# Performance work log

Measured on AMD Instinct MI355X. Metric: run time of the kernel, lower is better.

Reference implementation:

```python
import jax, jax.numpy as jnp
import numpy as np

B, H, L, C = 16, 512, 4096, 1
LAM = 0.001  # kernel squash threshold (lam in LongConvKernel)


def setup_inputs() -> dict:
    key = jax.random.key(0)
    ks = jax.random.split(key, 5)
    u = jax.random.normal(ks[0], (B, H, L), jnp.float32)
    # LongConvKernel 'double_exp' init: K ~ N(0, 0.02^2) * exp(-(j/L) * (H//2)^(i/H))
    K = jax.random.normal(ks[1], (C, H, L), jnp.float32) * 0.02
    i = jnp.arange(H, dtype=jnp.float32)[:, None]
    j = jnp.arange(L, dtype=jnp.float32)[None, :]
    double_exp = jnp.exp(-(j / L) * jnp.power(float(H // 2), i / H))  # (H, L)
    kernel = K * double_exp[None]
    D = jax.random.normal(ks[2], (C, H), jnp.float32)  # skip connection params
    # TransposedLinear(C*H -> H): weight (d_output, d_input), kaiming-ish scale
    Wout = jax.random.normal(ks[3], (H, C * H), jnp.float32) / np.sqrt(C * H)
    bout = jax.random.normal(ks[4], (H,), jnp.float32) * 0.01
    return {"u": u, "kernel": kernel, "D": D, "Wout": Wout, "bout": bout}


def reference(u, kernel, D, Wout, bout):
    Lseq = u.shape[-1]
    # kernel squashing: relu(|k| - lam) * sign(k)  (soft-threshold)
    k = jax.nn.relu(jnp.abs(kernel) - LAM) * jnp.sign(kernel)  # (C, H, L)
    n = 2 * Lseq
    k_f = jnp.fft.rfft(k, n=n, axis=-1)            # (C, H, n//2+1) complex
    u_f = jnp.fft.rfft(u, n=n, axis=-1)            # (B, H, n//2+1) complex
    y_f = jnp.einsum('bhl,chl->bchl', u_f, k_f)    # pointwise multiply in freq
    y = jnp.fft.irfft(y_f, n=n, axis=-1)[..., :Lseq]  # (B, C, H, L)
    y = y + jnp.einsum('bhl,ch->bchl', u, D)       # skip term
    y = y.reshape(y.shape[0], C * H, Lseq)         # (B, C*H, L)
    y = jax.nn.gelu(y, approximate=False)          # activation (torch GELU = exact)
    # output_linear: TransposedLinear + swish postact
    y = jnp.einsum('bul,vu->bvl', y, Wout) + bout[None, :, None]
    y = jax.nn.silu(y)
    return y
```

## Files before the change

### kernel.cpp

```cpp
#include <hip/hip_runtime.h>
#include <hip/hip_bf16.h>
#include <math.h>

#define BB 16
#define HH 512
#define LL 4096
#define NFFT 8192
#define LAM 0.001f

typedef __attribute__((ext_vector_type(8))) short short8;
typedef __attribute__((ext_vector_type(4))) float floatx4;

__device__ __forceinline__ void cmul(float ar, float ai, float br, float bi,
                                     float& cr, float& ci) {
  cr = ar * br - ai * bi;
  ci = ar * bi + ai * br;
}

constexpr float W16C[10] = {1.f, 0.92387953f, 0.70710678f, 0.38268343f, 0.f,
                            -0.38268343f, -0.70710678f, -0.92387953f, -1.f, -0.92387953f};
constexpr float W16S[10] = {0.f, -0.38268343f, -0.70710678f, -0.92387953f, -1.f,
                            -0.92387953f, -0.70710678f, -0.38268343f, 0.f, 0.38268343f};
constexpr float W32C[16] = {1.f, 0.98078528f, 0.92387953f, 0.83146961f, 0.70710678f,
                            0.55557023f, 0.38268343f, 0.19509032f, 0.f, -0.19509032f,
                            -0.38268343f, -0.55557023f, -0.70710678f, -0.83146961f,
                            -0.92387953f, -0.98078528f};
constexpr float W32S[16] = {0.f, -0.19509032f, -0.38268343f, -0.55557023f, -0.70710678f,
                            -0.83146961f, -0.92387953f, -0.98078528f, -1.f, -0.98078528f,
                            -0.92387953f, -0.83146961f, -0.70710678f, -0.55557023f,
                            -0.38268343f, -0.19509032f};

__device__ __forceinline__ void fft16_f(float* xr, float* xi) {
  float yr[16], yi[16];
#pragma unroll
  for (int j = 0; j < 4; ++j) {
    float t0r = xr[j] + xr[j + 8],      t0i = xi[j] + xi[j + 8];
    float t1r = xr[j] - xr[j + 8],      t1i = xi[j] - xi[j + 8];
    float t2r = xr[j + 4] + xr[j + 12], t2i = xi[j + 4] + xi[j + 12];
    float t3r = xr[j + 4] - xr[j + 12], t3i = xi[j + 4] - xi[j + 12];
    float o0r = t0r + t2r, o0i = t0i + t2i;
    float o1r = t1r + t3i, o1i = t1i - t3r;
    float o2r = t0r - t2r, o2i = t0i - t2i;
    float o3r = t1r - t3i, o3i = t1i + t3r;
    yr[j] = o0r; yi[j] = o0i;
    if (j == 0) {
      yr[4] = o1r; yi[4] = o1i; yr[8] = o2r; yi[8] = o2i; yr[12] = o3r; yi[12] = o3i;
    } else {
      cmul(o1r, o1i, W16C[j], W16S[j], yr[j + 4], yi[j + 4]);
      cmul(o2r, o2i, W16C[2 * j], W16S[2 * j], yr[j + 8], yi[j + 8]);
      cmul(o3r, o3i, W16C[3 * j], W16S[3 * j], yr[j + 12], yi[j + 12]);
    }
  }
#pragma unroll
  for (int m = 0; m < 4; ++m) {
    float t0r = yr[4 * m] + yr[4 * m + 2],     t0i = yi[4 * m] + yi[4 * m + 2];
    float t1r = yr[4 * m] - yr[4 * m + 2],     t1i = yi[4 * m] - yi[4 * m + 2];
    float t2r = yr[4 * m + 1] + yr[4 * m + 3], t2i = yi[4 * m + 1] + yi[4 * m + 3];
    float t3r = yr[4 * m + 1] - yr[4 * m + 3], t3i = yi[4 * m + 1] - yi[4 * m + 3];
    xr[m] = t0r + t2r;       xi[m] = t0i + t2i;
    xr[m + 4] = t1r + t3i;   xi[m + 4] = t1i - t3r;
    xr[m + 8] = t0r - t2r;   xi[m + 8] = t0i - t2i;
    xr[m + 12] = t1r - t3i;  xi[m + 12] = t1i + t3r;
  }
}

__device__ __forceinline__ void ifft16_f(float* xr, float* xi) {
  float yr[16], yi[16];
#pragma unroll
  for (int m = 0; m < 4; ++m) {
    float t0r = xr[m] + xr[m + 8],      t0i = xi[m] + xi[m + 8];
    float t1r = xr[m] - xr[m + 8],      t1i = xi[m] - xi[m + 8];
    float t2r = xr[m + 4] + xr[m + 12], t2i = xi[m + 4] + xi[m + 12];
    float t3r = xr[m + 4] - xr[m + 12], t3i = xi[m + 4] - xi[m + 12];
    yr[4 * m] = t0r + t2r;     yi[4 * m] = t0i + t2i;
    yr[4 * m + 1] = t1r - t3i; yi[4 * m + 1] = t1i + t3r;
    yr[4 * m + 2] = t0r - t2r; yi[4 * m + 2] = t0i - t2i;
    yr[4 * m + 3] = t1r + t3i; yi[4 * m + 3] = t1i - t3r;
  }
#pragma unroll
  for (int j = 0; j < 4; ++j) {
    float v0r = yr[j], v0i = yi[j];
    float v1r, v1i, v2r, v2i, v3r, v3i;
    if (j == 0) {
      v1r = yr[4]; v1i = yi[4]; v2r = yr[8]; v2i = yi[8]; v3r = yr[12]; v3i = yi[12];
    } else {
      cmul(yr[j + 4], yi[j + 4], W16C[j], -W16S[j], v1r, v1i);
      cmul(yr[j + 8], yi[j + 8], W16C[2 * j], -W16S[2 * j], v2r, v2i);
      cmul(yr[j + 12], yi[j + 12], W16C[3 * j], -W16S[3 * j], v3r, v3i);
    }
    float t0r = v0r + v2r, t0i = v0i + v2i;
    float t1r = v0r - v2r, t1i = v0i - v2i;
    float t2r = v1r + v3r, t2i = v1i + v3i;
    float t3r = v1r - v3r, t3i = v1i - v3i;
    xr[j] = t0r + t2r;       xi[j] = t0i + t2i;
    xr[j + 4] = t1r - t3i;   xi[j + 4] = t1i + t3r;
    xr[j + 8] = t0r - t2r;   xi[j + 8] = t0i - t2i;
    xr[j + 12] = t1r + t3i;  xi[j + 12] = t1i - t3r;
  }
}

__device__ __forceinline__ void twtree(float ang, float* wc, float* ws) {
  wc[0] = 1.f; ws[0] = 0.f;
  __sincosf(ang, &ws[1], &wc[1]);
  cmul(wc[1], ws[1], wc[1], ws[1], wc[2], ws[2]);
  cmul(wc[1], ws[1], wc[2], ws[2], wc[3], ws[3]);
  cmul(wc[2], ws[2], wc[2], ws[2], wc[4], ws[4]);
  cmul(wc[1], ws[1], wc[4], ws[4], wc[5], ws[5]);
  cmul(wc[2], ws[2], wc[4], ws[4], wc[6], ws[6]);
  cmul(wc[3], ws[3], wc[4], ws[4], wc[7], ws[7]);
  cmul(wc[4], ws[4], wc[4], ws[4], wc[8], ws[8]);
#pragma unroll
  for (int m = 9; m < 16; ++m)
    cmul(wc[m - 8], ws[m - 8], wc[8], ws[8], wc[m], ws[m]);
}

__device__ __forceinline__ float gelu_exact(float y) {
  return 0.5f * y * (1.f + erff(y * 0.70710678118654752f));
}

__global__ void wconv_kernel(const float* __restrict__ W,
                             __hip_bfloat16* __restrict__ Wb) {
  int i = blockIdx.x * 256 + threadIdx.x;
  Wb[i] = __float2bfloat16(W[i]);
}

__global__ __launch_bounds__(512)
__attribute__((amdgpu_waves_per_eu(4, 4)))
void kf_kernel(const float* __restrict__ kern, float* __restrict__ Kf) {
  __shared__ __align__(16) float sre[NFFT];
  __shared__ __align__(16) float sim[NFFT];
  const int t = threadIdx.x;
  const int h = blockIdx.x;
  const float* kr = kern + (size_t)h * LL;

  {
    const int j = t;
    float xr[16], xi[16];
#pragma unroll
    for (int r = 0; r < 8; ++r) {
      float kv = kr[j + 512 * r];
      float a = fabsf(kv) - LAM;
      float sq = (a > 0.f) ? ((kv > 0.f) ? a : -a) : 0.f;
      xr[r] = sq * (1.0f / (float)NFFT);
      xi[r] = 0.f;
    }
#pragma unroll
    for (int r = 8; r < 16; ++r) { xr[r] = 0.f; xi[r] = 0.f; }
    fft16_f(xr, xi);
    float wc[16], ws[16];
    twtree(-6.283185307179586f * (float)j * (1.f / 8192.f), wc, ws);
    const int jx = j ^ (((j >> 5) & 7) << 2);
#pragma unroll
    for (int m = 0; m < 16; ++m) {
      float tr, ti; cmul(xr[m], xi[m], wc[m], ws[m], tr, ti);
      sre[jx + 512 * m] = tr; sim[jx + 512 * m] = ti;
    }
  }
  __syncthreads();

  {
    const int jj = t & 31, gg = t >> 5;
    const int base = gg * 512 + jj;
    float xr[16], xi[16];
#pragma unroll
    for (int m = 0; m < 16; ++m) {
      const int a = (base + 32 * m) ^ ((m & 7) << 2);
      xr[m] = sre[a]; xi[m] = sim[a];
    }
    fft16_f(xr, xi);
    float wc[16], ws[16];
    twtree(-6.283185307179586f * (float)jj * (1.f / 512.f), wc, ws);
#pragma unroll
    for (int m = 0; m < 16; ++m) {
      const int a = (base + 32 * m) ^ ((m & 7) << 2);
      float tr, ti; cmul(xr[m], xi[m], wc[m], ws[m], tr, ti);
      sre[a] = tr; sim[a] = ti;
    }
  }
  __syncthreads();

  {
    const int k = t >> 1, par = t & 1;
    const int kx = k & 7;
    const float sgn = par ? -1.f : 1.f;
    float xr[16], xi[16];
#pragma unroll
    for (int c = 0; c < 4; ++c) {
      float4 lr = ((const float4*)sre)[8 * k + (c ^ kx)];
      float4 hr = ((const float4*)sre)[8 * k + ((c + 4) ^ kx)];
      float4 li = ((const float4*)sim)[8 * k + (c ^ kx)];
      float4 hi4 = ((const float4*)sim)[8 * k + ((c + 4) ^ kx)];
      float vr[4] = {lr.x + sgn * hr.x, lr.y + sgn * hr.y, lr.z + sgn * hr.z, lr.w + sgn * hr.w};
      float vi[4] = {li.x + sgn * hi4.x, li.y + sgn * hi4.y, li.z + sgn * hi4.z, li.w + sgn * hi4.w};
#pragma unroll
      for (int e = 0; e < 4; ++e) {
        const int j = 4 * c + e;
        const float twr = par ? W32C[j] : 1.f;
        const float tws = par ? W32S[j] : 0.f;
        cmul(vr[e], vi[e], twr, tws, xr[j], xi[j]);
      }
    }
    fft16_f(xr, xi);
    float4* out4 = (float4*)(Kf + (size_t)h * NFFT * 2) + 8 * t;
#pragma unroll
    for (int c = 0; c < 8; ++c)
      out4[c] = make_float4(xr[2 * c], xi[2 * c], xr[2 * c + 1], xi[2 * c + 1]);
  }
}

__global__ __launch_bounds__(512)
__attribute__((amdgpu_waves_per_eu(4, 4)))
void fftconv_kernel(
    const float* __restrict__ u, const float* __restrict__ D,
    const float* __restrict__ Kf, __hip_bfloat16* __restrict__ g) {
  __shared__ __align__(16) float sre[NFFT];
  __shared__ __align__(16) float sim[NFFT];
  const int t = threadIdx.x;
  const int h = blockIdx.x;
  const int p = blockIdx.y;
  const int b0 = 2 * p, b1 = 2 * p + 1;
  const float* u0 = u + ((size_t)(b0 * HH + h)) * LL;
  const float* u1 = u + ((size_t)(b1 * HH + h)) * LL;

  float us0[8], us1[8];
  const int jx = t ^ (((t >> 5) & 7) << 2);

  {
    const int j = t;
    float xr[16], xi[16];
#pragma unroll
    for (int r = 0; r < 8; ++r) {
      float a = u0[j + 512 * r];
      float b = u1[j + 512 * r];
      us0[r] = a; us1[r] = b;
      xr[r] = a; xi[r] = b;
    }
#pragma unroll
    for (int r = 8; r < 16; ++r) { xr[r] = 0.f; xi[r] = 0.f; }
    fft16_f(xr, xi);
    float wc[16], ws[16];
    twtree(-6.283185307179586f * (float)j * (1.f / 8192.f), wc, ws);
#pragma unroll
    for (int m = 0; m < 16; ++m) {
      float tr, ti; cmul(xr[m], xi[m], wc[m], ws[m], tr, ti);
      sre[jx + 512 * m] = tr; sim[jx + 512 * m] = ti;
    }
  }
  __syncthreads();

  {
    const int jj = t & 31, gg = t >> 5;
    const int base = gg * 512 + jj;
    float xr[16], xi[16];
#pragma unroll
    for (int m = 0; m < 16; ++m) {
      const int a = (base + 32 * m) ^ ((m & 7) << 2);
      xr[m] = sre[a]; xi[m] = sim[a];
    }
    fft16_f(xr, xi);
    float wc[16], ws[16];
    twtree(-6.283185307179586f * (float)jj * (1.f / 512.f), wc, ws);
#pragma unroll
    for (int m = 0; m < 16; ++m) {
      const int a = (base + 32 * m) ^ ((m & 7) << 2);
      float tr, ti; cmul(xr[m], xi[m], wc[m], ws[m], tr, ti);
      sre[a] = tr; sim[a] = ti;
    }
  }
  __syncthreads();

  {
    const int k = t >> 1, par = t & 1;
    const int kx = k & 7;
    const float sgn = par ? -1.f : 1.f;
    float xr[16], xi[16];
#pragma unroll
    for (int c = 0; c < 4; ++c) {
      float4 lr = ((const float4*)sre)[8 * k + (c ^ kx)];
      float4 hr = ((const float4*)sre)[8 * k + ((c + 4) ^ kx)];
      float4 li = ((const float4*)sim)[8 * k + (c ^ kx)];
      float4 hi4 = ((const float4*)sim)[8 * k + ((c + 4) ^ kx)];
      float vr[4] = {lr.x + sgn * hr.x, lr.y + sgn * hr.y, lr.z + sgn * hr.z, lr.w + sgn * hr.w};
      float vi[4] = {li.x + sgn * hi4.x, li.y + sgn * hi4.y, li.z + sgn * hi4.z, li.w + sgn * hi4.w};
#pragma unroll
      for (int e = 0; e < 4; ++e) {
        const int j = 4 * c + e;
        const float twr = par ? W32C[j] : 1.f;
        const float tws = par ? W32S[j] : 0.f;
        cmul(vr[e], vi[e], twr, tws, xr[j], xi[j]);
      }
    }
    fft16_f(xr, xi);
    const float4* kf4 = (const float4*)(Kf + (size_t)h * NFFT * 2) + 8 * t;
#pragma unroll
    for (int c = 0; c < 8; ++c) {
      float4 kk = kf4[c];
      float tr, ti;
      cmul(xr[2 * c], xi[2 * c], kk.x, kk.y, tr, ti);
      xr[2 * c] = tr; xi[2 * c] = ti;
      cmul(xr[2 * c + 1], xi[2 * c + 1], kk.z, kk.w, tr, ti);
      xr[2 * c + 1] = tr; xi[2 * c + 1] = ti;
    }
    ifft16_f(xr, xi);
    float outr[16], outi[16];
#pragma unroll
    for (int j = 0; j < 16; ++j) {
      float pr, pi;
      if (par) cmul(xr[j], xi[j], W32C[j], -W32S[j], pr, pi);
      else { pr = xr[j]; pi = xi[j]; }
      float qr = __shfl_xor(pr, 1);
      float qi = __shfl_xor(pi, 1);
      outr[j] = par ? (qr - pr) : (pr + qr);
      outi[j] = par ? (qi - pi) : (pi + qi);
    }
#pragma unroll
    for (int c = 0; c < 4; ++c) {
      const int q = (4 * par + c) ^ kx;
      ((float4*)sre)[8 * k + q] = make_float4(outr[4 * c], outr[4 * c + 1], outr[4 * c + 2], outr[4 * c + 3]);
      ((float4*)sim)[8 * k + q] = make_float4(outi[4 * c], outi[4 * c + 1], outi[4 * c + 2], outi[4 * c + 3]);
    }
  }
  __syncthreads();

  {
    const int jj = t & 31, gg = t >> 5;
    const int base = gg * 512 + jj;
    float wc[16], ws[16];
    twtree(6.283185307179586f * (float)jj * (1.f / 512.f), wc, ws);
    float yr[16], yi[16];
#pragma unroll
    for (int m = 0; m < 16; ++m) {
      const int a = (base + 32 * m) ^ ((m & 7) << 2);
      cmul(sre[a], sim[a], wc[m], ws[m], yr[m], yi[m]);
    }
    ifft16_f(yr, yi);
#pragma unroll
    for (int m = 0; m < 16; ++m) {
      const int a = (base + 32 * m) ^ ((m & 7) << 2);
      sre[a] = yr[m]; sim[a] = yi[m];
    }
  }
  __syncthreads();

  {
    const int j = t;
    float wc[16], ws[16];
    twtree(6.283185307179586f * (float)j * (1.f / 8192.f), wc, ws);
    float yr[16], yi[16];
#pragma unroll
    for (int m = 0; m < 16; ++m) {
      cmul(sre[jx + 512 * m], sim[jx + 512 * m], wc[m], ws[m], yr[m], yi[m]);
    }
    ifft16_f(yr, yi);
    const float Dh = D[h];
    __hip_bfloat16* g0 = g + ((size_t)(b0 * HH + h)) * LL;
    __hip_bfloat16* g1 = g + ((size_t)(b1 * HH + h)) * LL;
#pragma unroll
    for (int r = 0; r < 8; ++r) {
      float y0 = yr[r] + Dh * us0[r];
      float y1 = yi[r] + Dh * us1[r];
      g0[j + 512 * r] = __float2bfloat16(gelu_exact(y0));
      g1[j + 512 * r] = __float2bfloat16(gelu_exact(y1));
    }
  }
}

__global__ __launch_bounds__(256) void transpose_kernel(
    const __hip_bfloat16* __restrict__ g, __hip_bfloat16* __restrict__ g2) {
  __shared__ unsigned short tile[64][72];
  const int lb = blockIdx.x;
  const int hb = blockIdx.y;
  const int b = blockIdx.z;
  const int l0 = lb * 64, h0 = hb * 64;
  const int tid = threadIdx.x;
  const int r = tid >> 3;
  const int gc = tid & 7;
  const int c = gc * 8;
  const unsigned short* gs = (const unsigned short*)g;
  unsigned short* g2s = (unsigned short*)g2;
  for (int it = 0; it < 2; ++it) {
    int rr = r + it * 32;
    int4 v = *(const int4*)(gs + ((size_t)(b * HH + h0 + rr)) * LL + l0 + c);
    *(int4*)&tile[rr][(gc ^ (rr >> 3)) << 3] = v;
  }
  __syncthreads();
  for (int it = 0; it < 2; ++it) {
    int rr = r + it * 32;
    const int pc = (rr & 7) | (((rr >> 3) ^ gc) << 3);
    unsigned short vals[8];
#pragma unroll
    for (int j = 0; j < 8; ++j) vals[j] = tile[c + j][pc];
    *(int4*)(g2s + ((size_t)(b * LL + l0 + rr)) * HH + h0 + c) = *(int4*)vals;
  }
}

__global__ __launch_bounds__(256, 4) void gemm_kernel(
    const __hip_bfloat16* __restrict__ Wb, const __hip_bfloat16* __restrict__ g2,
    const float* __restrict__ bout, float* __restrict__ out) {
  const int vt = blockIdx.x;
  const int lt = blockIdx.y;
  const int b = blockIdx.z;
  const int wave = threadIdx.x >> 6;
  const int ln = threadIdx.x & 63;
  const int wr = wave >> 1, wc = wave & 1;
  const int vbase = vt * 128 + wr * 64;
  const int lbase = lt * 128 + wc * 64;
  const int lane16 = ln & 15;
  const int quad = ln >> 4;

  floatx4 acc[4][4];
#pragma unroll
  for (int mi = 0; mi < 4; ++mi)
#pragma unroll
    for (int ni = 0; ni < 4; ++ni) acc[mi][ni] = (floatx4){0.f, 0.f, 0.f, 0.f};

  const unsigned short* A = (const unsigned short*)Wb;
  const unsigned short* Bm = (const unsigned short*)g2 + (size_t)b * LL * HH;

  for (int k0 = 0; k0 < HH; k0 += 32) {
    const int kk = k0 + quad * 8;
    short8 af[4], bf[4];
#pragma unroll
    for (int mi = 0; mi < 4; ++mi) {
      const int m = vbase + mi * 16 + lane16;
      af[mi] = *(const short8*)(A + (size_t)m * HH + kk);
    }
#pragma unroll
    for (int ni = 0; ni < 4; ++ni) {
      const int n = lbase + ni * 16 + lane16;
      bf[ni] = *(const short8*)(Bm + (size_t)n * HH + kk);
    }
#pragma unroll
    for (int mi = 0; mi < 4; ++mi)
#pragma unroll
      for (int ni = 0; ni < 4; ++ni)
        acc[mi][ni] = __builtin_amdgcn_mfma_f32_16x16x32_bf16(af[mi], bf[ni],
                                                              acc[mi][ni], 0, 0, 0);
  }

#pragma unroll
  for (int mi = 0; mi < 4; ++mi) {
#pragma unroll
    for (int r = 0; r < 4; ++r) {
      const int m = vbase + mi * 16 + quad * 4 + r;
      const float bias = bout[m];
#pragma unroll
      for (int ni = 0; ni < 4; ++ni) {
        const int n = lbase + ni * 16 + lane16;
        float y = acc[mi][ni][r] + bias;
        y = y / (1.f + __expf(-y));
        out[((size_t)(b * HH + m)) * LL + n] = y;
      }
    }
  }
}

extern "C" void kernel_launch(void* const* d_in, const int* in_sizes, int n_in,
                              void* d_out, int out_size, void* d_ws, size_t ws_size,
                              hipStream_t stream) {
  const float* u = (const float*)d_in[0];
  const float* kern = (const float*)d_in[1];
  const float* D = (const float*)d_in[2];
  const float* Wout = (const float*)d_in[3];
  const float* bout = (const float*)d_in[4];
  float* out = (float*)d_out;

  char* ws = (char*)d_ws;
  const size_t KF_BYTES = (size_t)HH * NFFT * sizeof(float2);
  const size_t G_BYTES = (size_t)BB * HH * LL * 2;
  float* Kf = (float*)ws;
  __hip_bfloat16* g = (__hip_bfloat16*)(ws + KF_BYTES);
  __hip_bfloat16* g2 = (__hip_bfloat16*)(ws + KF_BYTES + G_BYTES);
  __hip_bfloat16* Wb = (__hip_bfloat16*)(ws + KF_BYTES + 2 * G_BYTES);

  wconv_kernel<<<dim3((HH * HH) / 256), dim3(256), 0, stream>>>(Wout, Wb);
  kf_kernel<<<dim3(HH), dim3(512), 0, stream>>>(kern, Kf);
  fftconv_kernel<<<dim3(HH, BB / 2), dim3(512), 0, stream>>>(u, D, Kf, g);
  transpose_kernel<<<dim3(LL / 64, HH / 64, BB), dim3(256), 0, stream>>>(g, g2);
  gemm_kernel<<<dim3(HH / 128, LL / 128, BB), dim3(256), 0, stream>>>(Wb, g2, bout, out);
}
```

Measured before the change: 574.2 us.

## Precompute FFT twiddle tables and fold skip term into kernel spectrum

A small kernel now precomputes the twiddle factors into global tables, and the FFT kernels read them instead of building them per thread from sincos and complex-multiply chains. The D skip connection is folded into the kernel spectrum as a constant added to the real part (D/N), so fftconv no longer keeps u values in registers or adds D*u at the end. The waves_per_eu attribute is also removed. This lowers register pressure and ALU work but adds global/L2 loads of twiddles, and reuses the g2 buffer as scratch for the tables before the transpose overwrites it.

```diff
diff --git a/kernel.cpp b/kernel.cpp
--- a/kernel.cpp
+++ b/kernel.cpp
@@ -99,23 +99,25 @@
   }
 }
 
-__device__ __forceinline__ void twtree(float ang, float* wc, float* ws) {
-  wc[0] = 1.f; ws[0] = 0.f;
-  __sincosf(ang, &ws[1], &wc[1]);
-  cmul(wc[1], ws[1], wc[1], ws[1], wc[2], ws[2]);
-  cmul(wc[1], ws[1], wc[2], ws[2], wc[3], ws[3]);
-  cmul(wc[2], ws[2], wc[2], ws[2], wc[4], ws[4]);
-  cmul(wc[1], ws[1], wc[4], ws[4], wc[5], ws[5]);
-  cmul(wc[2], ws[2], wc[4], ws[4], wc[6], ws[6]);
-  cmul(wc[3], ws[3], wc[4], ws[4], wc[7], ws[7]);
-  cmul(wc[4], ws[4], wc[4], ws[4], wc[8], ws[8]);
-#pragma unroll
-  for (int m = 9; m < 16; ++m)
-    cmul(wc[m - 8], ws[m - 8], wc[8], ws[8], wc[m], ws[m]);
-}
-
 __device__ __forceinline__ float gelu_exact(float y) {
   return 0.5f * y * (1.f + erff(y * 0.70710678118654752f));
+}
+
+__global__ __launch_bounds__(512) void twgen_kernel(float4* __restrict__ tw1,
+                                                    float4* __restrict__ tw2) {
+  const int j = threadIdx.x;
+  const int m2 = blockIdx.x;
+  float s0, c0, s1, c1;
+  const float a1 = -6.283185307179586f / 8192.f;
+  sincosf(a1 * (float)(j * (2 * m2)), &s0, &c0);
+  sincosf(a1 * (float)(j * (2 * m2 + 1)), &s1, &c1);
+  tw1[m2 * 512 + j] = make_float4(c0, s0, c1, s1);
+  if (j < 32) {
+    const float a2 = -6.283185307179586f / 512.f;
+    sincosf(a2 * (float)(j * (2 * m2)), &s0, &c0);
+    sincosf(a2 * (float)(j * (2 * m2 + 1)), &s1, &c1);
+    tw2[m2 * 32 + j] = make_float4(c0, s0, c1, s1);
+  }
 }
 
 __global__ void wconv_kernel(const float* __restrict__ W,
@@ -125,8 +127,9 @@
 }
 
 __global__ __launch_bounds__(512)
-__attribute__((amdgpu_waves_per_eu(4, 4)))
-void kf_kernel(const float* __restrict__ kern, float* __restrict__ Kf) {
+void kf_kernel(const float* __restrict__ kern, const float* __restrict__ D,
+               float* __restrict__ Kf, const float4* __restrict__ tw1,
+               const float4* __restrict__ tw2) {
   __shared__ __align__(16) float sre[NFFT];
   __shared__ __align__(16) float sim[NFFT];
   const int t = threadIdx.x;
@@ -147,13 +150,15 @@
 #pragma unroll
     for (int r = 8; r < 16; ++r) { xr[r] = 0.f; xi[r] = 0.f; }
     fft16_f(xr, xi);
-    float wc[16], ws[16];
-    twtree(-6.283185307179586f * (float)j * (1.f / 8192.f), wc, ws);
     const int jx = j ^ (((j >> 5) & 7) << 2);
 #pragma unroll
-    for (int m = 0; m < 16; ++m) {
-      float tr, ti; cmul(xr[m], xi[m], wc[m], ws[m], tr, ti);
-      sre[jx + 512 * m] = tr; sim[jx + 512 * m] = ti;
+    for (int m2 = 0; m2 < 8; ++m2) {
+      float4 w = tw1[m2 * 512 + j];
+      float tr, ti;
+      cmul(xr[2 * m2], xi[2 * m2], w.x, w.y, tr, ti);
+      sre[jx + 512 * (2 * m2)] = tr; sim[jx + 512 * (2 * m2)] = ti;
+      cmul(xr[2 * m2 + 1], xi[2 * m2 + 1], w.z, w.w, tr, ti);
+      sre[jx + 512 * (2 * m2 + 1)] = tr; sim[jx + 512 * (2 * m2 + 1)] = ti;
     }
   }
   __syncthreads();
@@ -168,13 +173,16 @@
       xr[m] = sre[a]; xi[m] = sim[a];
     }
     fft16_f(xr, xi);
-    float wc[16], ws[16];
-    twtree(-6.283185307179586f * (float)jj * (1.f / 512.f), wc, ws);
-#pragma unroll
-    for (int m = 0; m < 16; ++m) {
-      const int a = (base + 32 * m) ^ ((m & 7) << 2);
-      float tr, ti; cmul(xr[m], xi[m], wc[m], ws[m], tr, ti);
-      sre[a] = tr; sim[a] = ti;
+#pragma unroll
+    for (int m2 = 0; m2 < 8; ++m2) {
+      float4 w = tw2[m2 * 32 + jj];
+      float tr, ti;
+      int a0 = (base + 32 * (2 * m2)) ^ (((2 * m2) & 7) << 2);
+      cmul(xr[2 * m2], xi[2 * m2], w.x, w.y, tr, ti);
+      sre[a0] = tr; sim[a0] = ti;
+      int a1 = (base + 32 * (2 * m2 + 1)) ^ (((2 * m2 + 1) & 7) << 2);
+      cmul(xr[2 * m2 + 1], xi[2 * m2 + 1], w.z, w.w, tr, ti);
+      sre[a1] = tr; sim[a1] = ti;
     }
   }
   __syncthreads();
@@ -201,18 +209,19 @@
       }
     }
     fft16_f(xr, xi);
+    const float dsc = D[h] * (1.0f / (float)NFFT);
     float4* out4 = (float4*)(Kf + (size_t)h * NFFT * 2) + 8 * t;
 #pragma unroll
     for (int c = 0; c < 8; ++c)
-      out4[c] = make_float4(xr[2 * c], xi[2 * c], xr[2 * c + 1], xi[2 * c + 1]);
+      out4[c] = make_float4(xr[2 * c] + dsc, xi[2 * c], xr[2 * c + 1] + dsc, xi[2 * c + 1]);
   }
 }
 
 __global__ __launch_bounds__(512)
-__attribute__((amdgpu_waves_per_eu(4, 4)))
 void fftconv_kernel(
-    const float* __restrict__ u, const float* __restrict__ D,
-    const float* __restrict__ Kf, __hip_bfloat16* __restrict__ g) {
+    const float* __restrict__ u, const float* __restrict__ Kf,
+    __hip_bfloat16* __restrict__ g, const float4* __restrict__ tw1,
+    const float4* __restrict__ tw2) {
   __shared__ __align__(16) float sre[NFFT];
   __shared__ __align__(16) float sim[NFFT];
   const int t = threadIdx.x;
@@ -222,7 +231,6 @@
   const float* u0 = u + ((size_t)(b0 * HH + h)) * LL;
   const float* u1 = u + ((size_t)(b1 * HH + h)) * LL;
 
-  float us0[8], us1[8];
   const int jx = t ^ (((t >> 5) & 7) << 2);
 
   {
@@ -230,20 +238,20 @@
     float xr[16], xi[16];
 #pragma unroll
     for (int r = 0; r < 8; ++r) {
-      float a = u0[j + 512 * r];
-      float b = u1[j + 512 * r];
-      us0[r] = a; us1[r] = b;
-      xr[r] = a; xi[r] = b;
+      xr[r] = u0[j + 512 * r];
+      xi[r] = u1[j + 512 * r];
     }
 #pragma unroll
     for (int r = 8; r < 16; ++r) { xr[r] = 0.f; xi[r] = 0.f; }
     fft16_f(xr, xi);
-    float wc[16], ws[16];
-    twtree(-6.283185307179586f * (float)j * (1.f / 8192.f), wc, ws);
-#pragma unroll
-    for (int m = 0; m < 16; ++m) {
-      float tr, ti; cmul(xr[m], xi[m], wc[m], ws[m], tr, ti);
-      sre[jx + 512 * m] = tr; sim[jx + 512 * m] = ti;
+#pragma unroll
+    for (int m2 = 0; m2 < 8; ++m2) {
+      float4 w = tw1[m2 * 512 + j];
+      float tr, ti;
+      cmul(xr[2 * m2], xi[2 * m2], w.x, w.y, tr, ti);
+      sre[jx + 512 * (2 * m2)] = tr; sim[jx + 512 * (2 * m2)] = ti;
+      cmul(xr[2 * m2 + 1], xi[2 * m2 + 1], w.z, w.w, tr, ti);
+      sre[jx + 512 * (2 * m2 + 1)] = tr; sim[jx + 512 * (2 * m2 + 1)] = ti;
     }
   }
   __syncthreads();
@@ -258,13 +266,16 @@
       xr[m] = sre[a]; xi[m] = sim[a];
     }
     fft16_f(xr, xi);
-    float wc[16], ws[16];
-    twtree(-6.283185307179586f * (float)jj * (1.f / 512.f), wc, ws);
-#pragma unroll
-    for (int m = 0; m < 16; ++m) {
-      const int a = (base + 32 * m) ^ ((m & 7) << 2);
-      float tr, ti; cmul(xr[m], xi[m], wc[m], ws[m], tr, ti);
-      sre[a] = tr; sim[a] = ti;
+#pragma unroll
+    for (int m2 = 0; m2 < 8; ++m2) {
+      float4 w = tw2[m2 * 32 + jj];
+      float tr, ti;
+      int a0 = (base + 32 * (2 * m2)) ^ (((2 * m2) & 7) << 2);
+      cmul(xr[2 * m2], xi[2 * m2], w.x, w.y, tr, ti);
+      sre[a0] = tr; sim[a0] = ti;
+      int a1 = (base + 32 * (2 * m2 + 1)) ^ (((2 * m2 + 1) & 7) << 2);
+      cmul(xr[2 * m2 + 1], xi[2 * m2 + 1], w.z, w.w, tr, ti);
+      sre[a1] = tr; sim[a1] = ti;
     }
   }
   __syncthreads();
@@ -325,13 +336,14 @@
   {
     const int jj = t & 31, gg = t >> 5;
     const int base = gg * 512 + jj;
-    float wc[16], ws[16];
-    twtree(6.283185307179586f * (float)jj * (1.f / 512.f), wc, ws);
     float yr[16], yi[16];
 #pragma unroll
-    for (int m = 0; m < 16; ++m) {
-      const int a = (base + 32 * m) ^ ((m & 7) << 2);
-      cmul(sre[a], sim[a], wc[m], ws[m], yr[m], yi[m]);
+    for (int m2 = 0; m2 < 8; ++m2) {
+      float4 w = tw2[m2 * 32 + jj];
+      int a0 = (base + 32 * (2 * m2)) ^ (((2 * m2) & 7) << 2);
+      cmul(sre[a0], sim[a0], w.x, -w.y, yr[2 * m2], yi[2 * m2]);
+      int a1 = (base + 32 * (2 * m2 + 1)) ^ (((2 * m2 + 1) & 7) << 2);
+      cmul(sre[a1], sim[a1], w.z, -w.w, yr[2 * m2 + 1], yi[2 * m2 + 1]);
     }
     ifft16_f(yr, yi);
 #pragma unroll
@@ -344,23 +356,22 @@
 
   {
     const int j = t;
-    float wc[16], ws[16];
-    twtree(6.283185307179586f * (float)j * (1.f / 8192.f), wc, ws);
     float yr[16], yi[16];
 #pragma unroll
-    for (int m = 0; m < 16; ++m) {
-      cmul(sre[jx + 512 * m], sim[jx + 512 * m], wc[m], ws[m], yr[m], yi[m]);
+    for (int m2 = 0; m2 < 8; ++m2) {
+      float4 w = tw1[m2 * 512 + j];
+      cmul(sre[jx + 512 * (2 * m2)], sim[jx + 512 * (2 * m2)], w.x, -w.y,
+           yr[2 * m2], yi[2 * m2]);
+      cmul(sre[jx + 512 * (2 * m2 + 1)], sim[jx + 512 * (2 * m2 + 1)], w.z, -w.w,
+           yr[2 * m2 + 1], yi[2 * m2 + 1]);
     }
     ifft16_f(yr, yi);
-    const float Dh = D[h];
     __hip_bfloat16* g0 = g + ((size_t)(b0 * HH + h)) * LL;
     __hip_bfloat16* g1 = g + ((size_t)(b1 * HH + h)) * LL;
 #pragma unroll
     for (int r = 0; r < 8; ++r) {
-      float y0 = yr[r] + Dh * us0[r];
-      float y1 = yi[r] + Dh * us1[r];
-      g0[j + 512 * r] = __float2bfloat16(gelu_exact(y0));
-      g1[j + 512 * r] = __float2bfloat16(gelu_exact(y1));
+      g0[j + 512 * r] = __float2bfloat16(gelu_exact(yr[r]));
+      g1[j + 512 * r] = __float2bfloat16(gelu_exact(yi[r]));
     }
   }
 }
@@ -472,10 +483,13 @@
   __hip_bfloat16* g = (__hip_bfloat16*)(ws + KF_BYTES);
   __hip_bfloat16* g2 = (__hip_bfloat16*)(ws + KF_BYTES + G_BYTES);
   __hip_bfloat16* Wb = (__hip_bfloat16*)(ws + KF_BYTES + 2 * G_BYTES);
-
+  float4* tw1 = (float4*)g2;
+  float4* tw2 = tw1 + 8 * 512;
+
+  twgen_kernel<<<dim3(8), dim3(512), 0, stream>>>(tw1, tw2);
   wconv_kernel<<<dim3((HH * HH) / 256), dim3(256), 0, stream>>>(Wout, Wb);
-  kf_kernel<<<dim3(HH), dim3(512), 0, stream>>>(kern, Kf);
-  fftconv_kernel<<<dim3(HH, BB / 2), dim3(512), 0, stream>>>(u, D, Kf, g);
+  kf_kernel<<<dim3(HH), dim3(512), 0, stream>>>(kern, D, Kf, tw1, tw2);
+  fftconv_kernel<<<dim3(HH, BB / 2), dim3(512), 0, stream>>>(u, Kf, g, tw1, tw2);
   transpose_kernel<<<dim3(LL / 64, HH / 64, BB), dim3(256), 0, stream>>>(g, g2);
   gemm_kernel<<<dim3(HH / 128, LL / 128, BB), dim3(256), 0, stream>>>(Wb, g2, bout, out);
 }
```

After: 588.8 us. 2.5% more time.
